# Kernel tuning notes

Hardware: AMD Instinct MI355X
Metric: run time of the kernel (lower is better)

## Reference

```python
import jax, jax.numpy as jnp
import numpy as np

DRN = 0.4
TWO_PI = 2.0 * np.pi


def _mlp(x, ws, bs):
    # torch_geometric MLP with act='LeakyRelu' (slope 0.01), dropout=0 (eval), norm treated as identity (eval running stats)
    for w, b in zip(ws[:-1], bs[:-1]):
        x = jax.nn.leaky_relu(x @ w + b, 0.01)
    return x @ ws[-1] + bs[-1]


def _conv(x, ws, bs):
    # x: [B, N, F] = [pt, h..., ang_re, ang_im]. Dense masked equivalent of radius-graph EdgeConv.
    ang = x[..., -2:]
    d2 = jnp.sum((ang[:, :, None, :] - ang[:, None, :, :]) ** 2, -1)
    adj = (d2 <= DRN * DRN).astype(x.dtype)  # [B,N,N], i=target, j=source, self-loops included (radius ball)
    h = x[..., 1:-2]
    B, N, H = h.shape
    hi = jnp.broadcast_to(h[:, :, None, :], (B, N, N, H))
    hj = jnp.broadcast_to(h[:, None, :, :], (B, N, N, H))
    re, im = ang[..., 0], ang[..., 1]
    r2 = re * re + im * im
    nrm = jnp.maximum(jnp.sqrt(r2[:, :, None] * r2[:, None, :]), 1e-12)
    cos = (re[:, :, None] * re[:, None, :] + im[:, :, None] * im[:, None, :]) / nrm
    sin = (im[:, :, None] * re[:, None, :] - re[:, :, None] * im[:, None, :]) / nrm
    feat = jnp.concatenate([hi, hj, hj - hi, cos[..., None], sin[..., None]], -1)
    m = _mlp(feat, ws, bs)  # [B,N,N,H_out+1]
    # pt-weighted aggregation: message pt is the TARGET's pt (x_i[:, :1] in torch code)
    pt = x[..., 0]
    msg_pt = pt[:, :, None] * adj
    denom = jnp.sum(msg_pt, -1, keepdims=True)
    w = jnp.where(denom > 0, msg_pt / denom, 0.0)  # nan_to_num equivalent
    agg = jnp.einsum('bij,bijk->bik', w, m)
    sw = jnp.sum(w, -1)
    agg_pt = pt * sw                      # sum_j w * pt_i
    agg_ang = ang * sw[..., None]          # sum_j w * ang_i
    # phase renormalization: exp(2*pi*i*gamma) * (re + i*im)
    gamma = agg[..., -1]
    c, s = jnp.cos(TWO_PI * gamma), jnp.sin(TWO_PI * gamma)
    re2 = c * agg_ang[..., 0] - s * agg_ang[..., 1]
    im2 = s * agg_ang[..., 0] + c * agg_ang[..., 1]
    return jnp.concatenate([agg_pt[..., None], agg[..., :-1], re2[..., None], im2[..., None]], -1)


def _forward(pt, angles, c0w, c0b, c1w, c1b, rw, rb):
    absz = jnp.sqrt(jnp.sum(angles ** 2, -1))  # |view_as_complex(angles)|
    x = jnp.concatenate([pt[..., None], absz[..., None], angles], -1)
    x = _conv(x, c0w, c0b)
    x = _conv(x, c1w, c1b)
    # pt-weighted readout over particles
    ptf = x[..., 0]
    denom = jnp.sum(ptf, -1, keepdims=True)
    wj = jnp.where(denom > 0, ptf / denom, 0.0)
    xg = jnp.einsum('bn,bnf->bf', wj, x[..., 1:])
    logits = _mlp(xg[:, :-2], rw, rb)
    return jnp.concatenate([jax.nn.sigmoid(logits), xg[:, -2:]], -1)


def setup_inputs() -> dict:
    key = jax.random.key(0)
    ks = jax.random.split(key, 16)
    B, N = 128, 128
    pt = jax.random.uniform(ks[0], (B, N), jnp.float32, 0.05, 1.0)  # all > 0 so mask is all-true
    angles = 0.25 * jax.random.normal(ks[1], (B, N, 2), jnp.float32)

    def lin(k, i, o):
        return (0.2 / np.sqrt(i)) * jax.random.normal(k, (i, o), jnp.float32) * np.sqrt(i)

    H = 16
    return {
        'pt': pt, 'angles': angles,
        'c0_w0': lin(ks[2], 5, H), 'c0_b0': jnp.zeros((H,), jnp.float32),
        'c0_w1': lin(ks[3], H, H + 1), 'c0_b1': jnp.zeros((H + 1,), jnp.float32),
        'c1_w0': lin(ks[4], 3 * H + 2, H), 'c1_b0': jnp.zeros((H,), jnp.float32),
        'c1_w1': lin(ks[5], H, H + 1), 'c1_b1': jnp.zeros((H + 1,), jnp.float32),
        'r_w0': lin(ks[6], H, 32), 'r_b0': jnp.zeros((32,), jnp.float32),
        'r_w1': lin(ks[7], 32, 32), 'r_b1': jnp.zeros((32,), jnp.float32),
        'r_w2': lin(ks[8], 32, 1), 'r_b2': jnp.zeros((1,), jnp.float32),
    }


def reference(pt, angles, c0_w0, c0_b0, c0_w1, c0_b1, c1_w0, c1_b0, c1_w1, c1_b1, r_w0, r_b0, r_w1, r_b1, r_w2, r_b2):
    return _forward(pt, angles, (c0_w0, c0_w1), (c0_b0, c0_b1), (c1_w0, c1_w1), (c1_b0, c1_b1), (r_w0, r_w1, r_w2), (r_b0, r_b1, r_b2))
```

## Files before the change

kernel.cpp:

```cpp
#include <hip/hip_runtime.h>
#include <math.h>


#define BB 128
#define NN 128
#define BN (BB * NN)

typedef float f32x2 __attribute__((ext_vector_type(2)));

__device__ __forceinline__ f32x2 pk2(float s) { f32x2 r; r[0] = s; r[1] = s; return r; }
__device__ __forceinline__ f32x2 pkfma(f32x2 a, f32x2 b, f32x2 c) {
    return __builtin_elementwise_fma(a, b, c);
}
__device__ __forceinline__ f32x2 pkmax(f32x2 a, f32x2 b) {
    return __builtin_elementwise_max(a, b);
}

template <int CTRL>
__device__ __forceinline__ float dpp_add(float x) {
    int tmp = __builtin_amdgcn_update_dpp(0, __float_as_int(x), CTRL, 0xF, 0xF, true);
    return x + __int_as_float(tmp);
}

__device__ __forceinline__ float grp16_sum(float x) {
    x = dpp_add<0xB1>(x);
    x = dpp_add<0x4E>(x);
    x = dpp_add<0x114>(x);
    x = dpp_add<0x118>(x);
    return x;
}

__device__ __forceinline__ float bcast_grp(float x, int bidx) {
    return __int_as_float(__builtin_amdgcn_ds_bpermute(bidx, __float_as_int(x)));
}

__device__ __forceinline__ f32x2 grp16_red2(f32x2 x, int bidx) {
    f32x2 r;
    r[0] = bcast_grp(grp16_sum(x[0]), bidx);
    r[1] = bcast_grp(grp16_sum(x[1]), bidx);
    return r;
}

__global__ __launch_bounds__(256, 4) void conv0_kernel(
    const float* __restrict__ ang,
    const float* __restrict__ w0,
    const float* __restrict__ b0,
    const float* __restrict__ w1,
    const float* __restrict__ b1,
    const float* __restrict__ nw0,
    const float* __restrict__ nb0,
    float* __restrict__ ang1,
    float* __restrict__ u1,
    float* __restrict__ v1)
{
    const int tid  = threadIdx.x;
    const int lane = tid & 63;
    const int wid  = tid >> 6;
    const int t    = lane & 15;
    const int g    = lane >> 4;
    const int ni   = blockIdx.x * 16 + wid * 4 + g;
    const int base = (blockIdx.x >> 3) << 7;

    __shared__ float hls[16][20];

    const float2 ai = ((const float2*)ang)[ni];
    const float r2i = fmaf(ai.x, ai.x, ai.y * ai.y);
    const float abszi = __builtin_amdgcn_sqrtf(r2i);
    const float invi  = __builtin_amdgcn_rsqf(r2i);

    float2 ajv[8];
    #pragma unroll
    for (int jj = 0; jj < 8; ++jj)
        ajv[jj] = ((const float2*)ang)[base + jj * 16 + t];

    f32x2 u0b2[8], q02[8], wc2[8], ws2[8];
    #pragma unroll
    for (int p = 0; p < 8; ++p) {
        f32x2 wa  = *(const f32x2*)(w0 + 2 * p);
        f32x2 wb  = *(const f32x2*)(w0 + 16 + 2 * p);
        f32x2 wcv = *(const f32x2*)(w0 + 32 + 2 * p);
        f32x2 bb  = *(const f32x2*)(b0 + 2 * p);
        u0b2[p] = pkfma(pk2(abszi), wa - wcv, bb);
        q02[p]  = wb + wcv;
        wc2[p]  = *(const f32x2*)(w0 + 48 + 2 * p);
        ws2[p]  = *(const f32x2*)(w0 + 64 + 2 * p);
    }

    float w1row[16], w1g[16];
    #pragma unroll
    for (int k = 0; k < 16; ++k) {
        w1row[k] = w1[k * 17 + t];
        w1g[k]   = w1[k * 17 + 16];
    }
    const float b1t = b1[t], b1g = b1[16];

    const int o   = lane & 31;
    const int kk  = o & 15;
    const bool isU = (o < 16);
    float wk[16];
    {
        const int off = isU ? 0 : 256;
        #pragma unroll
        for (int c = 0; c < 16; ++c) {
            float a_ = nw0[off + c * 16 + kk];
            float c_ = nw0[512 + c * 16 + kk];
            wk[c] = isU ? (a_ - c_) : (a_ + c_);
        }
    }
    const float accb = isU ? nb0[kk] : 0.0f;

    f32x2 A2[8];
    #pragma unroll
    for (int p = 0; p < 8; ++p) A2[p] = pk2(0.0f);
    float degf = 0.0f;

    #pragma unroll
    for (int jj = 0; jj < 8; ++jj) {
        const float2 aj = ajv[jj];
        const float r2j = fmaf(aj.x, aj.x, aj.y * aj.y);
        const float abszj = __builtin_amdgcn_sqrtf(r2j);
        const float ivj   = __builtin_amdgcn_rsqf(r2j);
        const float dre = ai.x - aj.x, dim = ai.y - aj.y;
        const float d2 = fmaf(dre, dre, dim * dim);
        const float adjf = (d2 <= 0.16f) ? 1.0f : 0.0f;
        degf += adjf;
        const float inv = fminf(invi * ivj, 1e12f);
        const f32x2 cos2 = pk2(fmaf(ai.x, aj.x, ai.y * aj.y) * inv);
        const f32x2 sin2 = pk2(fmaf(ai.y, aj.x, -(ai.x * aj.y)) * inv);
        const f32x2 ab2 = pk2(abszj);
        const f32x2 adj2 = pk2(adjf);
        #pragma unroll
        for (int p = 0; p < 8; ++p) {
            f32x2 z = pkfma(ab2, q02[p], u0b2[p]);
            z = pkfma(cos2, wc2[p], z);
            z = pkfma(sin2, ws2[p], z);
            f32x2 a = pkmax(z, z * 0.01f);
            A2[p] = pkfma(a, adj2, A2[p]);
        }
    }

    const int bidx = (lane | 15) << 2;
    f32x2 Ak2[8];
    #pragma unroll
    for (int p = 0; p < 8; ++p) Ak2[p] = grp16_red2(A2[p], bidx);
    const float invdeg = __builtin_amdgcn_rcpf(bcast_grp(grp16_sum(degf), bidx));

    f32x2 s2 = pk2(0.0f), g2 = pk2(0.0f);
    #pragma unroll
    for (int p = 0; p < 8; ++p) {
        f32x2 wr; wr[0] = w1row[2 * p]; wr[1] = w1row[2 * p + 1];
        f32x2 wg; wg[0] = w1g[2 * p];   wg[1] = w1g[2 * p + 1];
        s2 = pkfma(Ak2[p], wr, s2);
        g2 = pkfma(Ak2[p], wg, g2);
    }
    const float mt    = fmaf(s2[0] + s2[1], invdeg, b1t);
    const float gamma = fmaf(g2[0] + g2[1], invdeg, b1g);

    {
        const float gf = gamma - floorf(gamma);
        const float cs = __builtin_amdgcn_cosf(gf);
        const float sn = __builtin_amdgcn_sinf(gf);
        const float re2 = cs * ai.x - sn * ai.y;
        const float im2 = fmaf(sn, ai.x, cs * ai.y);
        if (t == 0) ((float4*)ang1)[ni] = make_float4(re2, im2, invi, 0.0f);
    }

    hls[wid * 4 + g][t] = mt;

    #pragma unroll
    for (int p = 0; p < 2; ++p) {
        const int nl = (lane >> 5) + 2 * p;
        const int node = wid * 4 + nl;
        float acc = accb;
        #pragma unroll
        for (int c = 0; c < 16; ++c) acc = fmaf(hls[node][c], wk[c], acc);
        const int nout = (blockIdx.x * 16 + node);
        if (isU) u1[nout * 16 + kk] = acc;
        else     v1[nout * 16 + kk] = acc;
    }
}

__global__ __launch_bounds__(256, 4) void conv1_kernel(
    const float* __restrict__ pt,
    const float* __restrict__ ang1,
    const float* __restrict__ u1,
    const float* __restrict__ v1,
    const float* __restrict__ w0,
    const float* __restrict__ w1,
    const float* __restrict__ b1,
    float* __restrict__ part)
{
    const int tid  = threadIdx.x;
    const int lane = tid & 63;
    const int wid  = tid >> 6;
    const int t    = lane & 15;
    const int g    = lane >> 4;
    const int ni   = blockIdx.x * 16 + wid * 4 + g;
    const int base = (blockIdx.x >> 3) << 7;

    const float4 a4 = ((const float4*)ang1)[ni];
    const float rei = a4.x, imi = a4.y, invi = a4.z;
    const float ptf = pt[ni];

    f32x2 u0b2[8], wc2[8], ws2[8];
    {
        const float4* ug = (const float4*)(u1 + (size_t)ni * 16);
        float4 q0 = ug[0], q1 = ug[1], q2 = ug[2], q3 = ug[3];
        u0b2[0][0] = q0.x; u0b2[0][1] = q0.y; u0b2[1][0] = q0.z; u0b2[1][1] = q0.w;
        u0b2[2][0] = q1.x; u0b2[2][1] = q1.y; u0b2[3][0] = q1.z; u0b2[3][1] = q1.w;
        u0b2[4][0] = q2.x; u0b2[4][1] = q2.y; u0b2[5][0] = q2.z; u0b2[5][1] = q2.w;
        u0b2[6][0] = q3.x; u0b2[6][1] = q3.y; u0b2[7][0] = q3.z; u0b2[7][1] = q3.w;
    }
    #pragma unroll
    for (int p = 0; p < 8; ++p) {
        wc2[p] = *(const f32x2*)(w0 + 768 + 2 * p);
        ws2[p] = *(const f32x2*)(w0 + 784 + 2 * p);
    }

    f32x2 A2[8];
    #pragma unroll
    for (int p = 0; p < 8; ++p) A2[p] = pk2(0.0f);
    float degf = 0.0f;

    #pragma unroll
    for (int jj = 0; jj < 8; ++jj) {
        const int j = base + jj * 16 + t;
        const float4 aj = ((const float4*)ang1)[j];
        f32x2 vj2[8];
        {
            const float4* vg = (const float4*)(v1 + (size_t)j * 16);
            float4 q0 = vg[0], q1 = vg[1], q2 = vg[2], q3 = vg[3];
            vj2[0][0] = q0.x; vj2[0][1] = q0.y; vj2[1][0] = q0.z; vj2[1][1] = q0.w;
            vj2[2][0] = q1.x; vj2[2][1] = q1.y; vj2[3][0] = q1.z; vj2[3][1] = q1.w;
            vj2[4][0] = q2.x; vj2[4][1] = q2.y; vj2[5][0] = q2.z; vj2[5][1] = q2.w;
            vj2[6][0] = q3.x; vj2[6][1] = q3.y; vj2[7][0] = q3.z; vj2[7][1] = q3.w;
        }
        const float dre = rei - aj.x, dim = imi - aj.y;
        const float d2 = fmaf(dre, dre, dim * dim);
        const float adjf = (d2 <= 0.16f) ? 1.0f : 0.0f;
        degf += adjf;
        const float inv = fminf(invi * aj.z, 1e12f);
        const f32x2 cos2 = pk2(fmaf(rei, aj.x, imi * aj.y) * inv);
        const f32x2 sin2 = pk2(fmaf(imi, aj.x, -(rei * aj.y)) * inv);
        const f32x2 adj2 = pk2(adjf);
        #pragma unroll
        for (int p = 0; p < 8; ++p) {
            f32x2 z = u0b2[p] + vj2[p];
            z = pkfma(cos2, wc2[p], z);
            z = pkfma(sin2, ws2[p], z);
            f32x2 a = pkmax(z, z * 0.01f);
            A2[p] = pkfma(a, adj2, A2[p]);
        }
    }

    const int bidx = (lane | 15) << 2;
    f32x2 Ak2[8];
    #pragma unroll
    for (int p = 0; p < 8; ++p) Ak2[p] = grp16_red2(A2[p], bidx);
    const float invdeg = __builtin_amdgcn_rcpf(bcast_grp(grp16_sum(degf), bidx));

    f32x2 s2 = pk2(0.0f), g2 = pk2(0.0f);
    #pragma unroll
    for (int p = 0; p < 8; ++p) {
        f32x2 wr; wr[0] = w1[(2 * p) * 17 + t];  wr[1] = w1[(2 * p + 1) * 17 + t];
        f32x2 wg; wg[0] = w1[(2 * p) * 17 + 16]; wg[1] = w1[(2 * p + 1) * 17 + 16];
        s2 = pkfma(Ak2[p], wr, s2);
        g2 = pkfma(Ak2[p], wg, g2);
    }
    const float mt    = fmaf(s2[0] + s2[1], invdeg, b1[t]);
    const float gamma = fmaf(g2[0] + g2[1], invdeg, b1[16]);

    const float gf = gamma - floorf(gamma);
    const float cs = __builtin_amdgcn_cosf(gf);
    const float sn = __builtin_amdgcn_sinf(gf);
    const float re2 = cs * rei - sn * imi;
    const float im2 = fmaf(sn, rei, cs * imi);

    float pm  = ptf * mt;
    float pre = ptf * re2;
    float pim = ptf * im2;
    float ppt = ptf;
    pm  += __int_as_float(__builtin_amdgcn_ds_swizzle(__float_as_int(pm),  0x401F));
    pre += __int_as_float(__builtin_amdgcn_ds_swizzle(__float_as_int(pre), 0x401F));
    pim += __int_as_float(__builtin_amdgcn_ds_swizzle(__float_as_int(pim), 0x401F));
    ppt += __int_as_float(__builtin_amdgcn_ds_swizzle(__float_as_int(ppt), 0x401F));
    pm  += __shfl_xor(pm, 32);
    pre += __shfl_xor(pre, 32);
    pim += __shfl_xor(pim, 32);
    ppt += __shfl_xor(ppt, 32);

    float* po = part + (size_t)(blockIdx.x * 4 + wid) * 20;
    if (lane < 16)       po[lane] = pm;
    else if (lane == 16) po[16] = pre;
    else if (lane == 17) po[17] = pim;
    else if (lane == 18) po[18] = ppt;
}

__global__ __launch_bounds__(64) void readout_kernel(
    const float* __restrict__ part,
    const float* __restrict__ w0, const float* __restrict__ b0,
    const float* __restrict__ w1, const float* __restrict__ b1,
    const float* __restrict__ w2, const float* __restrict__ b2,
    float* __restrict__ out) {
    const int b = blockIdx.x;
    const int t = threadIdx.x;

    __shared__ float sbuf[19];
    __shared__ float xg[18];
    __shared__ float h1r[32];

    if (t < 19) {
        float s0 = 0.0f, s1 = 0.0f, s2 = 0.0f, s3 = 0.0f;
        const float* pb = part + (size_t)b * 32 * 20 + t;
        #pragma unroll
        for (int r = 0; r < 32; r += 4) {
            s0 += pb[(r + 0) * 20];
            s1 += pb[(r + 1) * 20];
            s2 += pb[(r + 2) * 20];
            s3 += pb[(r + 3) * 20];
        }
        sbuf[t] = (s0 + s1) + (s2 + s3);
    }
    const float invd = __builtin_amdgcn_rcpf(sbuf[18]);
    if (t < 18) xg[t] = sbuf[t] * invd;

    if (t < 32) {
        float h = b0[t];
        #pragma unroll
        for (int k = 0; k < 16; ++k) h = fmaf(xg[k], w0[k * 32 + t], h);
        h = fmaxf(h, 0.01f * h);
        h1r[t] = h;
    }
    if (t < 32) {
        float h = b1[t];
        #pragma unroll
        for (int k = 0; k < 32; ++k) h = fmaf(h1r[k], w1[k * 32 + t], h);
        h = fmaxf(h, 0.01f * h);
        float p = h * w2[t];
        #pragma unroll
        for (int off = 16; off; off >>= 1) p += __shfl_xor(p, off);
        if (t == 0) {
            out[b * 3 + 0] = 1.0f / (1.0f + expf(-(p + b2[0])));
            out[b * 3 + 1] = xg[16];
            out[b * 3 + 2] = xg[17];
        }
    }
}

extern "C" void kernel_launch(void* const* d_in, const int* in_sizes, int n_in,
                              void* d_out, int out_size, void* d_ws, size_t ws_size,
                              hipStream_t stream) {
    const float* pt    = (const float*)d_in[0];
    const float* ang   = (const float*)d_in[1];
    const float* c0_w0 = (const float*)d_in[2];
    const float* c0_b0 = (const float*)d_in[3];
    const float* c0_w1 = (const float*)d_in[4];
    const float* c0_b1 = (const float*)d_in[5];
    const float* c1_w0 = (const float*)d_in[6];
    const float* c1_b0 = (const float*)d_in[7];
    const float* c1_w1 = (const float*)d_in[8];
    const float* c1_b1 = (const float*)d_in[9];
    const float* r_w0  = (const float*)d_in[10];
    const float* r_b0  = (const float*)d_in[11];
    const float* r_w1  = (const float*)d_in[12];
    const float* r_b1  = (const float*)d_in[13];
    const float* r_w2  = (const float*)d_in[14];
    const float* r_b2  = (const float*)d_in[15];
    float* out = (float*)d_out;
    float* ws = (float*)d_ws;

    float* ang1  = ws;
    float* u1    = ang1 + (size_t)BN * 4;
    float* v1    = u1 + (size_t)BN * 16;
    float* partb = v1 + (size_t)BN * 16;

    hipLaunchKernelGGL(conv0_kernel, dim3(BN / 16), dim3(256), 0, stream,
                       ang, c0_w0, c0_b0, c0_w1, c0_b1, c1_w0, c1_b0,
                       ang1, u1, v1);
    hipLaunchKernelGGL(conv1_kernel, dim3(BN / 16), dim3(256), 0, stream,
                       pt, ang1, u1, v1, c1_w0, c1_w1, c1_b1, partb);
    hipLaunchKernelGGL(readout_kernel, dim3(BB), dim3(64), 0, stream,
                       partb, r_w0, r_b0, r_w1, r_b1, r_w2, r_b2, out);
}
```

Before: 33.20 us.

## Fuse conv0 and conv1 into one kernel with per-batch LDS intermediates

Merges the two conv kernels into a single 1024-thread kernel: each block takes one batch-half, recomputes conv0 for all 128 nodes of the batch, and keeps the u/v projections and rotated angles in LDS instead of writing them to global memory. Conv1 then reads neighbour data from LDS, and per-wave partial sums are reduced in-block before being written out, so readout only adds two partials. This removes a kernel launch and the global round trip of the intermediates. In exchange conv0 work is duplicated across the two halves, and the 1024-thread blocks with larger LDS use may lower occupancy, with only 256 blocks in the grid.

```diff
diff --git a/kernel.cpp b/kernel.cpp
--- a/kernel.cpp
+++ b/kernel.cpp
@@ -41,7 +41,8 @@
     return r;
 }
 
-__global__ __launch_bounds__(256, 4) void conv0_kernel(
+__global__ __launch_bounds__(1024, 4) void fused_kernel(
+    const float* __restrict__ pt,
     const float* __restrict__ ang,
     const float* __restrict__ w0,
     const float* __restrict__ b0,
@@ -49,172 +50,166 @@
     const float* __restrict__ b1,
     const float* __restrict__ nw0,
     const float* __restrict__ nb0,
-    float* __restrict__ ang1,
-    float* __restrict__ u1,
-    float* __restrict__ v1)
+    const float* __restrict__ nw1,
+    const float* __restrict__ nb1,
+    float* __restrict__ part)
 {
-    const int tid  = threadIdx.x;
-    const int lane = tid & 63;
-    const int wid  = tid >> 6;
-    const int t    = lane & 15;
-    const int g    = lane >> 4;
-    const int ni   = blockIdx.x * 16 + wid * 4 + g;
-    const int base = (blockIdx.x >> 3) << 7;
-
-    __shared__ float hls[16][20];
-
-    const float2 ai = ((const float2*)ang)[ni];
-    const float r2i = fmaf(ai.x, ai.x, ai.y * ai.y);
-    const float abszi = __builtin_amdgcn_sqrtf(r2i);
-    const float invi  = __builtin_amdgcn_rsqf(r2i);
-
-    float2 ajv[8];
-    #pragma unroll
-    for (int jj = 0; jj < 8; ++jj)
-        ajv[jj] = ((const float2*)ang)[base + jj * 16 + t];
-
-    f32x2 u0b2[8], q02[8], wc2[8], ws2[8];
+    const int tid   = threadIdx.x;
+    const int lane  = tid & 63;
+    const int wid   = tid >> 6;
+    const int t     = lane & 15;
+    const int g     = lane >> 4;
+    const int batch = blockIdx.x >> 1;
+    const int ihalf = blockIdx.x & 1;
+    const int nbase = batch * NN;
+
+    __shared__ float u_lds[128][20];
+    __shared__ float v_lds[128][20];
+    __shared__ float4 rec_lds[128];
+    __shared__ float hls[64][20];
+    __shared__ float Ap2[16][20];
+
+    float2 ajv[8]; float abszj[8], ivjr[8];
+    #pragma unroll
+    for (int jj = 0; jj < 8; ++jj) {
+        ajv[jj] = ((const float2*)ang)[nbase + jj * 16 + t];
+        const float r2 = fmaf(ajv[jj].x, ajv[jj].x, ajv[jj].y * ajv[jj].y);
+        abszj[jj] = __builtin_amdgcn_sqrtf(r2);
+        ivjr[jj]  = __builtin_amdgcn_rsqf(r2);
+    }
+    f32x2 q02[8], wc2[8], ws2[8], wac2[8], bb2[8];
     #pragma unroll
     for (int p = 0; p < 8; ++p) {
         f32x2 wa  = *(const f32x2*)(w0 + 2 * p);
         f32x2 wb  = *(const f32x2*)(w0 + 16 + 2 * p);
         f32x2 wcv = *(const f32x2*)(w0 + 32 + 2 * p);
-        f32x2 bb  = *(const f32x2*)(b0 + 2 * p);
-        u0b2[p] = pkfma(pk2(abszi), wa - wcv, bb);
+        bb2[p]  = *(const f32x2*)(b0 + 2 * p);
+        wac2[p] = wa - wcv;
         q02[p]  = wb + wcv;
         wc2[p]  = *(const f32x2*)(w0 + 48 + 2 * p);
         ws2[p]  = *(const f32x2*)(w0 + 64 + 2 * p);
     }
 
-    float w1row[16], w1g[16];
-    #pragma unroll
-    for (int k = 0; k < 16; ++k) {
-        w1row[k] = w1[k * 17 + t];
-        w1g[k]   = w1[k * 17 + 16];
-    }
-    const float b1t = b1[t], b1g = b1[16];
-
-    const int o   = lane & 31;
-    const int kk  = o & 15;
+    const int o = lane & 31;
+    const int kk = o & 15;
     const bool isU = (o < 16);
-    float wk[16];
+    const int bidx = (lane | 15) << 2;
+
+    #pragma unroll
+    for (int r = 0; r < 2; ++r) {
+        const int nlr    = wid * 4 + g;
+        const int nlocal = r * 64 + nlr;
+        const int ni     = nbase + nlocal;
+
+        const float2 ai = ((const float2*)ang)[ni];
+        const float r2i = fmaf(ai.x, ai.x, ai.y * ai.y);
+        const float abszi = __builtin_amdgcn_sqrtf(r2i);
+        const float invi  = __builtin_amdgcn_rsqf(r2i);
+
+        f32x2 u0b2[8];
+        #pragma unroll
+        for (int p = 0; p < 8; ++p) u0b2[p] = pkfma(pk2(abszi), wac2[p], bb2[p]);
+
+        f32x2 A2[8];
+        #pragma unroll
+        for (int p = 0; p < 8; ++p) A2[p] = pk2(0.0f);
+        float degf = 0.0f;
+
+        #pragma unroll
+        for (int jj = 0; jj < 8; ++jj) {
+            const float2 aj = ajv[jj];
+            const float dre = ai.x - aj.x, dim = ai.y - aj.y;
+            const float d2 = fmaf(dre, dre, dim * dim);
+            const float adjf = (d2 <= 0.16f) ? 1.0f : 0.0f;
+            degf += adjf;
+            const float inv = fminf(invi * ivjr[jj], 1e12f);
+            const f32x2 cos2 = pk2(fmaf(ai.x, aj.x, ai.y * aj.y) * inv);
+            const f32x2 sin2 = pk2(fmaf(ai.y, aj.x, -(ai.x * aj.y)) * inv);
+            const f32x2 ab2 = pk2(abszj[jj]);
+            const f32x2 adj2 = pk2(adjf);
+            #pragma unroll
+            for (int p = 0; p < 8; ++p) {
+                f32x2 z = pkfma(ab2, q02[p], u0b2[p]);
+                z = pkfma(cos2, wc2[p], z);
+                z = pkfma(sin2, ws2[p], z);
+                f32x2 a = pkmax(z, z * 0.01f);
+                A2[p] = pkfma(a, adj2, A2[p]);
+            }
+        }
+
+        f32x2 Ak2[8];
+        #pragma unroll
+        for (int p = 0; p < 8; ++p) Ak2[p] = grp16_red2(A2[p], bidx);
+        const float invdeg = __builtin_amdgcn_rcpf(bcast_grp(grp16_sum(degf), bidx));
+
+        f32x2 s2 = pk2(0.0f), g2 = pk2(0.0f);
+        #pragma unroll
+        for (int p = 0; p < 8; ++p) {
+            f32x2 wr; wr[0] = w1[(2 * p) * 17 + t];  wr[1] = w1[(2 * p + 1) * 17 + t];
+            f32x2 wg; wg[0] = w1[(2 * p) * 17 + 16]; wg[1] = w1[(2 * p + 1) * 17 + 16];
+            s2 = pkfma(Ak2[p], wr, s2);
+            g2 = pkfma(Ak2[p], wg, g2);
+        }
+        const float mt    = fmaf(s2[0] + s2[1], invdeg, b1[t]);
+        const float gamma = fmaf(g2[0] + g2[1], invdeg, b1[16]);
+
+        {
+            const float gf = gamma - floorf(gamma);
+            const float cs = __builtin_amdgcn_cosf(gf);
+            const float sn = __builtin_amdgcn_sinf(gf);
+            if (t == 0) {
+                const float re2 = cs * ai.x - sn * ai.y;
+                const float im2 = fmaf(sn, ai.x, cs * ai.y);
+                rec_lds[nlocal] = make_float4(re2, im2, invi, 0.0f);
+            }
+        }
+
+        hls[nlr][t] = mt;
+
+        float wkp[16];
+        {
+            const int off = isU ? 0 : 256;
+            #pragma unroll
+            for (int c = 0; c < 16; ++c) {
+                const float a_ = nw0[off + c * 16 + kk];
+                const float c_ = nw0[512 + c * 16 + kk];
+                wkp[c] = isU ? (a_ - c_) : (a_ + c_);
+            }
+        }
+        const float accb = isU ? nb0[kk] : 0.0f;
+        #pragma unroll
+        for (int ps = 0; ps < 2; ++ps) {
+            const int nl = (lane >> 5) + 2 * ps;
+            const int node = wid * 4 + nl;
+            float acc = accb;
+            #pragma unroll
+            for (int c = 0; c < 16; ++c) acc = fmaf(hls[node][c], wkp[c], acc);
+            if (isU) u_lds[r * 64 + node][kk] = acc;
+            else     v_lds[r * 64 + node][kk] = acc;
+        }
+    }
+    __syncthreads();
+
+    const int nlocal1 = ihalf * 64 + wid * 4 + g;
+    const int ni1 = nbase + nlocal1;
+    const float4 a4 = rec_lds[nlocal1];
+    const float rei = a4.x, imi = a4.y, invi1 = a4.z;
+    const float ptf = pt[ni1];
+
+    f32x2 u0b2[8];
     {
-        const int off = isU ? 0 : 256;
-        #pragma unroll
-        for (int c = 0; c < 16; ++c) {
-            float a_ = nw0[off + c * 16 + kk];
-            float c_ = nw0[512 + c * 16 + kk];
-            wk[c] = isU ? (a_ - c_) : (a_ + c_);
-        }
-    }
-    const float accb = isU ? nb0[kk] : 0.0f;
-
-    f32x2 A2[8];
-    #pragma unroll
-    for (int p = 0; p < 8; ++p) A2[p] = pk2(0.0f);
-    float degf = 0.0f;
-
-    #pragma unroll
-    for (int jj = 0; jj < 8; ++jj) {
-        const float2 aj = ajv[jj];
-        const float r2j = fmaf(aj.x, aj.x, aj.y * aj.y);
-        const float abszj = __builtin_amdgcn_sqrtf(r2j);
-        const float ivj   = __builtin_amdgcn_rsqf(r2j);
-        const float dre = ai.x - aj.x, dim = ai.y - aj.y;
-        const float d2 = fmaf(dre, dre, dim * dim);
-        const float adjf = (d2 <= 0.16f) ? 1.0f : 0.0f;
-        degf += adjf;
-        const float inv = fminf(invi * ivj, 1e12f);
-        const f32x2 cos2 = pk2(fmaf(ai.x, aj.x, ai.y * aj.y) * inv);
-        const f32x2 sin2 = pk2(fmaf(ai.y, aj.x, -(ai.x * aj.y)) * inv);
-        const f32x2 ab2 = pk2(abszj);
-        const f32x2 adj2 = pk2(adjf);
-        #pragma unroll
-        for (int p = 0; p < 8; ++p) {
-            f32x2 z = pkfma(ab2, q02[p], u0b2[p]);
-            z = pkfma(cos2, wc2[p], z);
-            z = pkfma(sin2, ws2[p], z);
-            f32x2 a = pkmax(z, z * 0.01f);
-            A2[p] = pkfma(a, adj2, A2[p]);
-        }
-    }
-
-    const int bidx = (lane | 15) << 2;
-    f32x2 Ak2[8];
-    #pragma unroll
-    for (int p = 0; p < 8; ++p) Ak2[p] = grp16_red2(A2[p], bidx);
-    const float invdeg = __builtin_amdgcn_rcpf(bcast_grp(grp16_sum(degf), bidx));
-
-    f32x2 s2 = pk2(0.0f), g2 = pk2(0.0f);
-    #pragma unroll
-    for (int p = 0; p < 8; ++p) {
-        f32x2 wr; wr[0] = w1row[2 * p]; wr[1] = w1row[2 * p + 1];
-        f32x2 wg; wg[0] = w1g[2 * p];   wg[1] = w1g[2 * p + 1];
-        s2 = pkfma(Ak2[p], wr, s2);
-        g2 = pkfma(Ak2[p], wg, g2);
-    }
-    const float mt    = fmaf(s2[0] + s2[1], invdeg, b1t);
-    const float gamma = fmaf(g2[0] + g2[1], invdeg, b1g);
-
-    {
-        const float gf = gamma - floorf(gamma);
-        const float cs = __builtin_amdgcn_cosf(gf);
-        const float sn = __builtin_amdgcn_sinf(gf);
-        const float re2 = cs * ai.x - sn * ai.y;
-        const float im2 = fmaf(sn, ai.x, cs * ai.y);
-        if (t == 0) ((float4*)ang1)[ni] = make_float4(re2, im2, invi, 0.0f);
-    }
-
-    hls[wid * 4 + g][t] = mt;
-
-    #pragma unroll
-    for (int p = 0; p < 2; ++p) {
-        const int nl = (lane >> 5) + 2 * p;
-        const int node = wid * 4 + nl;
-        float acc = accb;
-        #pragma unroll
-        for (int c = 0; c < 16; ++c) acc = fmaf(hls[node][c], wk[c], acc);
-        const int nout = (blockIdx.x * 16 + node);
-        if (isU) u1[nout * 16 + kk] = acc;
-        else     v1[nout * 16 + kk] = acc;
-    }
-}
-
-__global__ __launch_bounds__(256, 4) void conv1_kernel(
-    const float* __restrict__ pt,
-    const float* __restrict__ ang1,
-    const float* __restrict__ u1,
-    const float* __restrict__ v1,
-    const float* __restrict__ w0,
-    const float* __restrict__ w1,
-    const float* __restrict__ b1,
-    float* __restrict__ part)
-{
-    const int tid  = threadIdx.x;
-    const int lane = tid & 63;
-    const int wid  = tid >> 6;
-    const int t    = lane & 15;
-    const int g    = lane >> 4;
-    const int ni   = blockIdx.x * 16 + wid * 4 + g;
-    const int base = (blockIdx.x >> 3) << 7;
-
-    const float4 a4 = ((const float4*)ang1)[ni];
-    const float rei = a4.x, imi = a4.y, invi = a4.z;
-    const float ptf = pt[ni];
-
-    f32x2 u0b2[8], wc2[8], ws2[8];
-    {
-        const float4* ug = (const float4*)(u1 + (size_t)ni * 16);
+        const float4* ug = (const float4*)&u_lds[nlocal1][0];
         float4 q0 = ug[0], q1 = ug[1], q2 = ug[2], q3 = ug[3];
         u0b2[0][0] = q0.x; u0b2[0][1] = q0.y; u0b2[1][0] = q0.z; u0b2[1][1] = q0.w;
         u0b2[2][0] = q1.x; u0b2[2][1] = q1.y; u0b2[3][0] = q1.z; u0b2[3][1] = q1.w;
         u0b2[4][0] = q2.x; u0b2[4][1] = q2.y; u0b2[5][0] = q2.z; u0b2[5][1] = q2.w;
         u0b2[6][0] = q3.x; u0b2[6][1] = q3.y; u0b2[7][0] = q3.z; u0b2[7][1] = q3.w;
     }
+    f32x2 wc1[8], ws1[8];
     #pragma unroll
     for (int p = 0; p < 8; ++p) {
-        wc2[p] = *(const f32x2*)(w0 + 768 + 2 * p);
-        ws2[p] = *(const f32x2*)(w0 + 784 + 2 * p);
+        wc1[p] = *(const f32x2*)(nw0 + 768 + 2 * p);
+        ws1[p] = *(const f32x2*)(nw0 + 784 + 2 * p);
     }
 
     f32x2 A2[8];
@@ -222,38 +217,37 @@
     for (int p = 0; p < 8; ++p) A2[p] = pk2(0.0f);
     float degf = 0.0f;
 
-    #pragma unroll
+    #pragma unroll 4
     for (int jj = 0; jj < 8; ++jj) {
-        const int j = base + jj * 16 + t;
-        const float4 aj = ((const float4*)ang1)[j];
+        const int j = jj * 16 + t;
+        const float4 rj = rec_lds[j];
         f32x2 vj2[8];
         {
-            const float4* vg = (const float4*)(v1 + (size_t)j * 16);
+            const float4* vg = (const float4*)&v_lds[j][0];
             float4 q0 = vg[0], q1 = vg[1], q2 = vg[2], q3 = vg[3];
             vj2[0][0] = q0.x; vj2[0][1] = q0.y; vj2[1][0] = q0.z; vj2[1][1] = q0.w;
             vj2[2][0] = q1.x; vj2[2][1] = q1.y; vj2[3][0] = q1.z; vj2[3][1] = q1.w;
             vj2[4][0] = q2.x; vj2[4][1] = q2.y; vj2[5][0] = q2.z; vj2[5][1] = q2.w;
             vj2[6][0] = q3.x; vj2[6][1] = q3.y; vj2[7][0] = q3.z; vj2[7][1] = q3.w;
         }
-        const float dre = rei - aj.x, dim = imi - aj.y;
+        const float dre = rei - rj.x, dim = imi - rj.y;
         const float d2 = fmaf(dre, dre, dim * dim);
         const float adjf = (d2 <= 0.16f) ? 1.0f : 0.0f;
         degf += adjf;
-        const float inv = fminf(invi * aj.z, 1e12f);
-        const f32x2 cos2 = pk2(fmaf(rei, aj.x, imi * aj.y) * inv);
-        const f32x2 sin2 = pk2(fmaf(imi, aj.x, -(rei * aj.y)) * inv);
+        const float inv = fminf(invi1 * rj.z, 1e12f);
+        const f32x2 cos2 = pk2(fmaf(rei, rj.x, imi * rj.y) * inv);
+        const f32x2 sin2 = pk2(fmaf(imi, rj.x, -(rei * rj.y)) * inv);
         const f32x2 adj2 = pk2(adjf);
         #pragma unroll
         for (int p = 0; p < 8; ++p) {
             f32x2 z = u0b2[p] + vj2[p];
-            z = pkfma(cos2, wc2[p], z);
-            z = pkfma(sin2, ws2[p], z);
+            z = pkfma(cos2, wc1[p], z);
+            z = pkfma(sin2, ws1[p], z);
             f32x2 a = pkmax(z, z * 0.01f);
             A2[p] = pkfma(a, adj2, A2[p]);
         }
     }
 
-    const int bidx = (lane | 15) << 2;
     f32x2 Ak2[8];
     #pragma unroll
     for (int p = 0; p < 8; ++p) Ak2[p] = grp16_red2(A2[p], bidx);
@@ -262,13 +256,13 @@
     f32x2 s2 = pk2(0.0f), g2 = pk2(0.0f);
     #pragma unroll
     for (int p = 0; p < 8; ++p) {
-        f32x2 wr; wr[0] = w1[(2 * p) * 17 + t];  wr[1] = w1[(2 * p + 1) * 17 + t];
-        f32x2 wg; wg[0] = w1[(2 * p) * 17 + 16]; wg[1] = w1[(2 * p + 1) * 17 + 16];
+        f32x2 wr; wr[0] = nw1[(2 * p) * 17 + t];  wr[1] = nw1[(2 * p + 1) * 17 + t];
+        f32x2 wg; wg[0] = nw1[(2 * p) * 17 + 16]; wg[1] = nw1[(2 * p + 1) * 17 + 16];
         s2 = pkfma(Ak2[p], wr, s2);
         g2 = pkfma(Ak2[p], wg, g2);
     }
-    const float mt    = fmaf(s2[0] + s2[1], invdeg, b1[t]);
-    const float gamma = fmaf(g2[0] + g2[1], invdeg, b1[16]);
+    const float mt    = fmaf(s2[0] + s2[1], invdeg, nb1[t]);
+    const float gamma = fmaf(g2[0] + g2[1], invdeg, nb1[16]);
 
     const float gf = gamma - floorf(gamma);
     const float cs = __builtin_amdgcn_cosf(gf);
@@ -289,11 +283,23 @@
     pim += __shfl_xor(pim, 32);
     ppt += __shfl_xor(ppt, 32);
 
-    float* po = part + (size_t)(blockIdx.x * 4 + wid) * 20;
-    if (lane < 16)       po[lane] = pm;
-    else if (lane == 16) po[16] = pre;
-    else if (lane == 17) po[17] = pim;
-    else if (lane == 18) po[18] = ppt;
+    if (lane < 16)       Ap2[wid][lane] = pm;
+    else if (lane == 16) Ap2[wid][16] = pre;
+    else if (lane == 17) Ap2[wid][17] = pim;
+    else if (lane == 18) Ap2[wid][18] = ppt;
+    __syncthreads();
+
+    if (wid == 0 && lane < 19) {
+        float s0 = 0.0f, s1 = 0.0f, s2_ = 0.0f, s3 = 0.0f;
+        #pragma unroll
+        for (int w = 0; w < 16; w += 4) {
+            s0 += Ap2[w + 0][lane];
+            s1 += Ap2[w + 1][lane];
+            s2_ += Ap2[w + 2][lane];
+            s3 += Ap2[w + 3][lane];
+        }
+        part[(size_t)blockIdx.x * 20 + lane] = (s0 + s1) + (s2_ + s3);
+    }
 }
 
 __global__ __launch_bounds__(64) void readout_kernel(
@@ -305,24 +311,13 @@
     const int b = blockIdx.x;
     const int t = threadIdx.x;
 
-    __shared__ float sbuf[19];
+    __shared__ float sb[19];
     __shared__ float xg[18];
     __shared__ float h1r[32];
 
-    if (t < 19) {
-        float s0 = 0.0f, s1 = 0.0f, s2 = 0.0f, s3 = 0.0f;
-        const float* pb = part + (size_t)b * 32 * 20 + t;
-        #pragma unroll
-        for (int r = 0; r < 32; r += 4) {
-            s0 += pb[(r + 0) * 20];
-            s1 += pb[(r + 1) * 20];
-            s2 += pb[(r + 2) * 20];
-            s3 += pb[(r + 3) * 20];
-        }
-        sbuf[t] = (s0 + s1) + (s2 + s3);
-    }
-    const float invd = __builtin_amdgcn_rcpf(sbuf[18]);
-    if (t < 18) xg[t] = sbuf[t] * invd;
+    if (t < 19) sb[t] = part[(size_t)(2 * b) * 20 + t] + part[(size_t)(2 * b) * 20 + 20 + t];
+    const float invd = __builtin_amdgcn_rcpf(sb[18]);
+    if (t < 18) xg[t] = sb[t] * invd;
 
     if (t < 32) {
         float h = b0[t];
@@ -367,18 +362,11 @@
     const float* r_w2  = (const float*)d_in[14];
     const float* r_b2  = (const float*)d_in[15];
     float* out = (float*)d_out;
-    float* ws = (float*)d_ws;
-
-    float* ang1  = ws;
-    float* u1    = ang1 + (size_t)BN * 4;
-    float* v1    = u1 + (size_t)BN * 16;
-    float* partb = v1 + (size_t)BN * 16;
-
-    hipLaunchKernelGGL(conv0_kernel, dim3(BN / 16), dim3(256), 0, stream,
-                       ang, c0_w0, c0_b0, c0_w1, c0_b1, c1_w0, c1_b0,
-                       ang1, u1, v1);
-    hipLaunchKernelGGL(conv1_kernel, dim3(BN / 16), dim3(256), 0, stream,
-                       pt, ang1, u1, v1, c1_w0, c1_w1, c1_b1, partb);
+    float* partb = (float*)d_ws;
+
+    hipLaunchKernelGGL(fused_kernel, dim3(2 * BB), dim3(1024), 0, stream,
+                       pt, ang, c0_w0, c0_b0, c0_w1, c0_b1,
+                       c1_w0, c1_b0, c1_w1, c1_b1, partb);
     hipLaunchKernelGGL(readout_kernel, dim3(BB), dim3(64), 0, stream,
                        partb, r_w0, r_b0, r_w1, r_b1, r_w2, r_b2, out);
 }
```

Result: slower. 35.28 us (+6.3%).
